# Kernel optimization log

Hardware: AMD Instinct MI355X
Metric: run time of the kernel (lower is better)

Reference implementation:

```python
import jax, jax.numpy as jnp
import numpy as np

WEIGHT_FACTOR = 1.0
N_CLUSTERS = 64


def setup_inputs() -> dict:
    key = jax.random.key(0)
    k1, k2, k3 = jax.random.split(key, 3)
    B, H, W = 128, 256, 256
    x = jax.random.uniform(k1, (B, H, W), dtype=jnp.float32)
    pattern_importance = jax.random.uniform(k2, (B, N_CLUSTERS), dtype=jnp.float32)
    # dense cluster map: value in [0, N_CLUSTERS) = cluster id; == N_CLUSTERS = unassigned (mask stays 1)
    cluster_id = jax.random.randint(k3, (H, W), 0, N_CLUSTERS + 1, dtype=jnp.int32)
    return {"x": x, "pattern_importance": pattern_importance, "cluster_id": cluster_id}


def reference(x, pattern_importance, cluster_id):
    # FFT2 over last two dims; torch fftshift with dim=None shifts ALL axes (incl. batch),
    # and jnp.fft.fftshift has the same default semantics.
    x_fft = jnp.fft.fftshift(jnp.fft.fft2(x))
    assigned = cluster_id < N_CLUSTERS                     # [H, W] bool
    cid = jnp.where(assigned, cluster_id, 0)               # safe gather index
    vals = pattern_importance[:, cid] * WEIGHT_FACTOR      # [B, H, W] gather-built mask values
    mask = jnp.where(assigned[None, :, :], vals, jnp.float32(1.0))
    x_reject = x_fft * mask
    x_ifft = jnp.abs(jnp.fft.ifft2(jnp.fft.ifftshift(x_reject)))
    x_diff = jnp.abs(x_ifft - x)
    x_new = jnp.stack([x, x_ifft, x_diff], axis=1)         # [B, 3, H, W]
    return (x_new, pattern_importance)
```

## Files before the change

### kernel.cpp

```cpp
#include <hip/hip_runtime.h>
#include <hip/hip_fp16.h>
#include <math.h>

#define BB 128
#define HH 256
#define WW 256
#define HW 65536
#define OUT_B_STRIDE 196608

__device__ __forceinline__ float2 cadd(float2 a, float2 b){ return make_float2(a.x+b.x, a.y+b.y); }
__device__ __forceinline__ float2 csub(float2 a, float2 b){ return make_float2(a.x-b.x, a.y-b.y); }

template<bool INV>
__device__ __forceinline__ float2 cmul_t(float2 a, float2 b){
  if (INV) return make_float2(a.x*b.x + a.y*b.y, a.y*b.x - a.x*b.y);
  return make_float2(a.x*b.x - a.y*b.y, a.x*b.y + a.y*b.x);
}

template<bool INV>
__device__ __forceinline__ void fft4(float2&a,float2&b,float2&c,float2&d){
  float2 t0 = cadd(a,c), t1 = csub(a,c);
  float2 t2 = cadd(b,d), t3 = csub(b,d);
  float2 t3r = INV ? make_float2(-t3.y, t3.x) : make_float2(t3.y, -t3.x);
  a = cadd(t0,t2);
  b = cadd(t1,t3r);
  c = csub(t0,t2);
  d = csub(t1,t3r);
}

template<bool INV>
__device__ __forceinline__ void fft16(float2 x[16]){
  #pragma unroll
  for (int j0=0;j0<4;++j0) fft4<INV>(x[j0], x[j0+4], x[j0+8], x[j0+12]);
  const float WR[10] = {1.f, 0.923879533f, 0.707106781f, 0.382683432f, 0.f,
                        0.f, -0.707106781f, 0.f, 0.f, -0.923879533f};
  const float WI[10] = {0.f, -0.382683432f, -0.707106781f, -0.923879533f, -1.f,
                        0.f, -0.707106781f, 0.f, 0.f, 0.382683432f};
  #pragma unroll
  for (int q0=1;q0<4;++q0)
    #pragma unroll
    for (int j0=1;j0<4;++j0){
      int k = j0*q0;
      x[j0+4*q0] = cmul_t<INV>(x[j0+4*q0], make_float2(WR[k], WI[k]));
    }
  #pragma unroll
  for (int q0=0;q0<4;++q0) fft4<INV>(x[4*q0], x[4*q0+1], x[4*q0+2], x[4*q0+3]);
  float2 t[16];
  #pragma unroll
  for (int q0=0;q0<4;++q0)
    #pragma unroll
    for (int q1=0;q1<4;++q1) t[q0+4*q1] = x[4*q0+q1];
  #pragma unroll
  for (int i=0;i<16;++i) x[i]=t[i];
}

__device__ __forceinline__ void build_tw256(float2* tw, int tid){
  float s,c;
  __sincosf(-6.28318530717958647692f * (float)tid / 256.0f, &s, &c);
  tw[tid] = make_float2(c, s);
}

__device__ __forceinline__ uint pkh2(float2 v){
  __half2 h = __float22half2_rn(v);
  return *(uint*)&h;
}
__device__ __forceinline__ float2 uph2(uint u){
  __half2 h = *(__half2*)&u;
  return __half22float2(h);
}

union SharedU {
  float  xs[16*272];
  float2 zbuf[16*273];
  float  ybuf[16*272];
};

__global__ __launch_bounds__(256, 4) void k_row_fwd(const float* __restrict__ x,
                                                    __half2* __restrict__ S,
                                                    const int* __restrict__ cid,
                                                    unsigned char* __restrict__ cidp){
  __shared__ SharedU sh;
  __shared__ float2 tw[256];
  int tid = threadIdx.x;
  int t = tid & 15, r = tid >> 4;
  build_tw256(tw, tid);

  if (blockIdx.x < 64){
    int g = (blockIdx.x*256 + tid) * 4;
    int p  = g >> 8;
    int s  = (g >> 4) & 15;
    int k1b = g & 15;
    int wfreq = 16*(p & 15) + (p >> 4);
    int w2 = (wfreq + 128) & 255;
    uchar4 v4;
    unsigned char* vp = (unsigned char*)&v4;
    #pragma unroll
    for (int i=0;i<4;++i){
      int h2 = (16*(k1b+i) + s + 128) & 255;
      int cv = cid[h2*256 + w2];
      vp[i] = (unsigned char)cv;
    }
    *(uchar4*)(cidp + g) = v4;
  }

  const float4* xb = (const float4*)x + (size_t)blockIdx.x * 1024;
  #pragma unroll
  for (int k=0;k<4;++k){
    int i2 = tid + k*256;
    float4 v = xb[i2];
    int row = i2 >> 6, c4 = i2 & 63;
    *(float4*)&sh.xs[row*272 + c4*4] = v;
  }
  __syncthreads();
  float2 X[16];
  #pragma unroll
  for (int j=0;j<16;++j) X[j] = make_float2(sh.xs[r*272 + 16*j + t], 0.f);
  __syncthreads();
  fft16<false>(X);
  #pragma unroll
  for (int q=0;q<16;++q) X[q] = cmul_t<false>(X[q], tw[t*q]);
  #pragma unroll
  for (int q=0;q<16;++q) sh.zbuf[r*273 + q*17 + t] = X[q];
  __syncthreads();
  float2 Y[16];
  #pragma unroll
  for (int tt=0;tt<16;++tt) Y[tt] = sh.zbuf[r*273 + t*17 + tt];
  fft16<false>(Y);
  int row = blockIdx.x*16 + r;
  int b = row >> 8, h = row & 255;
  uint4* dst = (uint4*)(S + (size_t)b*HW + h*256 + t*16);
  #pragma unroll
  for (int k=0;k<4;++k){
    uint4 q;
    q.x = pkh2(Y[4*k+0]); q.y = pkh2(Y[4*k+1]);
    q.z = pkh2(Y[4*k+2]); q.w = pkh2(Y[4*k+3]);
    dst[k] = q;
  }
}

__global__ __launch_bounds__(256, 4) void k_col(__half2* __restrict__ S,
                                                const unsigned char* __restrict__ cidp,
                                                const float* __restrict__ pi){
  __shared__ SharedU sh;
  __shared__ float2 tw[256];
  __shared__ float sPI[64];
  int tid = threadIdx.x;
  int c = tid & 15, t = tid >> 4;
  int cg = blockIdx.x, b = blockIdx.y;
  build_tw256(tw, tid);
  if (tid < 64) sPI[tid] = pi[(((b + 64) & 127) << 6) + tid] * 0.25f;
  __half2* Sb = S + (size_t)b*HW;
  int p = cg*16 + c;
  float2 X[16];
  #pragma unroll
  for (int j=0;j<16;++j) X[j] = uph2(*(uint*)&Sb[(16*j + t)*256 + p]);
  uint4 mq = *(const uint4*)(cidp + p*256 + t*16);
  __syncthreads();
  fft16<false>(X);
  #pragma unroll
  for (int q=0;q<16;++q) X[q] = cmul_t<false>(X[q], tw[t*q]);
  #pragma unroll
  for (int q=0;q<16;++q) sh.zbuf[c*273 + q*17 + t] = X[q];
  __syncthreads();
  int s = t;
  float2 Y[16];
  #pragma unroll
  for (int tt=0;tt<16;++tt) Y[tt] = sh.zbuf[c*273 + s*17 + tt];
  fft16<false>(Y);
  const uint* mw = (const uint*)&mq;
  #pragma unroll
  for (int k1=0;k1<16;++k1){
    int cv = (mw[k1>>2] >> ((k1&3)*8)) & 255;
    float m = (cv < 64) ? sPI[cv] : 0.25f;
    Y[k1].x *= m; Y[k1].y *= m;
  }
  __syncthreads();
  fft16<true>(Y);
  #pragma unroll
  for (int u=0;u<16;++u) Y[u] = cmul_t<true>(Y[u], tw[u*s]);
  #pragma unroll
  for (int u=0;u<16;++u) sh.zbuf[c*273 + u*17 + s] = Y[u];
  __syncthreads();
  float2 R[16];
  #pragma unroll
  for (int k0=0;k0<16;++k0) R[k0] = sh.zbuf[c*273 + t*17 + k0];
  fft16<true>(R);
  #pragma unroll
  for (int j=0;j<16;++j){
    uint u = pkh2(R[j]);
    *(uint*)&Sb[(16*j + t)*256 + p] = u;
  }
}

__global__ __launch_bounds__(256, 4) void k_row_inv_fused(const __half2* __restrict__ S,
                                                          const float* __restrict__ x,
                                                          const float* __restrict__ pi,
                                                          float* __restrict__ out){
  __shared__ SharedU sh;
  __shared__ float2 tw[256];
  int tid = threadIdx.x;
  int s = tid & 15, r = tid >> 4;
  int slice = blockIdx.x, b = blockIdx.y;
  build_tw256(tw, tid);
  int h = slice*16 + r;
  const uint4* src = (const uint4*)(S + (size_t)b*HW + h*256 + s*16);
  float2 X[16];
  #pragma unroll
  for (int k=0;k<4;++k){
    uint4 q = src[k];
    X[4*k+0] = uph2(q.x); X[4*k+1] = uph2(q.y);
    X[4*k+2] = uph2(q.z); X[4*k+3] = uph2(q.w);
  }
  __syncthreads();
  fft16<true>(X);
  #pragma unroll
  for (int u=0;u<16;++u) X[u] = cmul_t<true>(X[u], tw[u*s]);
  #pragma unroll
  for (int u=0;u<16;++u) sh.zbuf[r*273 + u*17 + s] = X[u];
  __syncthreads();
  float2 R[16];
  #pragma unroll
  for (int k0=0;k0<16;++k0) R[k0] = sh.zbuf[r*273 + s*17 + k0];
  fft16<true>(R);
  __syncthreads();
  const float scale = 1.0f/16384.0f;
  #pragma unroll
  for (int j=0;j<16;++j)
    sh.ybuf[r*272 + 16*j + s] = sqrtf(R[j].x*R[j].x + R[j].y*R[j].y) * scale;
  __syncthreads();
  const float4* x4 = (const float4*)x;
  float4* o4 = (float4*)out;
  size_t xbase = (size_t)b*16384 + slice*1024;
  size_t obase = (size_t)b*49152 + slice*1024;
  #pragma unroll
  for (int k=0;k<4;++k){
    int i2 = tid + k*256;
    int rr = i2 >> 6, c4 = i2 & 63;
    float4 y = *(float4*)&sh.ybuf[rr*272 + c4*4];
    float4 xv = x4[xbase + i2];
    float4 df;
    df.x = fabsf(y.x - xv.x); df.y = fabsf(y.y - xv.y);
    df.z = fabsf(y.z - xv.z); df.w = fabsf(y.w - xv.w);
    o4[obase + i2]         = xv;
    o4[obase + i2 + 16384] = y;
    o4[obase + i2 + 32768] = df;
  }
  if (slice == 0 && b < 8){
    const float4* p4 = (const float4*)pi;
    o4[6291456 + b*256 + tid] = p4[b*256 + tid];
  }
}

__global__ __launch_bounds__(256, 4) void k_row_inv_stage(const __half2* __restrict__ S,
                                                          float* __restrict__ out){
  __shared__ SharedU sh;
  __shared__ float2 tw[256];
  int tid = threadIdx.x;
  int s = tid & 15, r = tid >> 4;
  int slice = blockIdx.x, b = blockIdx.y;
  build_tw256(tw, tid);
  int h = slice*16 + r;
  const uint4* src = (const uint4*)(S + (size_t)b*HW + h*256 + s*16);
  float2 X[16];
  #pragma unroll
  for (int k=0;k<4;++k){
    uint4 q = src[k];
    X[4*k+0] = uph2(q.x); X[4*k+1] = uph2(q.y);
    X[4*k+2] = uph2(q.z); X[4*k+3] = uph2(q.w);
  }
  __syncthreads();
  fft16<true>(X);
  #pragma unroll
  for (int u=0;u<16;++u) X[u] = cmul_t<true>(X[u], tw[u*s]);
  #pragma unroll
  for (int u=0;u<16;++u) sh.zbuf[r*273 + u*17 + s] = X[u];
  __syncthreads();
  float2 R[16];
  #pragma unroll
  for (int k0=0;k0<16;++k0) R[k0] = sh.zbuf[r*273 + s*17 + k0];
  fft16<true>(R);
  const float scale = 1.0f/16384.0f;
  float* o = out + (size_t)b*OUT_B_STRIDE + h*256;
  #pragma unroll
  for (int j=0;j<16;++j)
    o[16*j + s] = sqrtf(R[j].x*R[j].x + R[j].y*R[j].y) * scale;
}

__global__ __launch_bounds__(256) void k_final(const float* __restrict__ x,
                                               const float* __restrict__ pi,
                                               float* __restrict__ out) {
  int i = blockIdx.x * 256 + threadIdx.x;
  const float4* x4 = (const float4*)x;
  float4* o4 = (float4*)out;
  int b = i >> 14;
  int r = i & 16383;
  int ch0 = b * 49152 + r;
  float4 y  = o4[ch0];
  float4 xv = x4[i];
  float4 df;
  df.x = fabsf(y.x - xv.x);
  df.y = fabsf(y.y - xv.y);
  df.z = fabsf(y.z - xv.z);
  df.w = fabsf(y.w - xv.w);
  o4[ch0]         = xv;
  o4[ch0 + 16384] = y;
  o4[ch0 + 32768] = df;
  if (i < 2048) {
    const float4* p4 = (const float4*)pi;
    o4[6291456 + i] = p4[i];
  }
}

extern "C" void kernel_launch(void* const* d_in, const int* in_sizes, int n_in,
                              void* d_out, int out_size, void* d_ws, size_t ws_size,
                              hipStream_t stream) {
  const float* x  = (const float*)d_in[0];
  const float* pi = (const float*)d_in[1];
  const int*  cid = (const int*)d_in[2];
  float* out = (float*)d_out;
  (void)in_sizes; (void)n_in; (void)out_size;

  const size_t S_bytes = (size_t)BB * HW * sizeof(__half2);
  const size_t cidp_bytes = 65536;

  if (ws_size >= S_bytes + cidp_bytes) {
    __half2* S = (__half2*)d_ws;
    unsigned char* cidp = (unsigned char*)d_ws + S_bytes;
    k_row_fwd<<<2048, 256, 0, stream>>>(x, S, cid, cidp);
    k_col<<<dim3(16, BB), 256, 0, stream>>>(S, cidp, pi);
    k_row_inv_fused<<<dim3(16, BB), 256, 0, stream>>>(S, x, pi, out);
  } else {
    __half2* S = (__half2*)((float*)out + HW);
    S = (__half2*)out + (size_t)BB * HW;
    unsigned char* cidp = (unsigned char*)d_ws;
    k_row_fwd<<<2048, 256, 0, stream>>>(x, S, cid, cidp);
    k_col<<<dim3(16, BB), 256, 0, stream>>>(S, cidp, pi);
    k_row_inv_stage<<<dim3(16, BB), 256, 0, stream>>>(S, out);
    k_final<<<8192, 256, 0, stream>>>(x, pi, out);
  }
}
```

Measured before the change: 176.3 us.

## Compute FFT twiddles in registers and stage transposes through half-precision LDS

Drops the shared-memory twiddle table and its build step in every FFT kernel. Twiddle factors are now made in registers from one sincos plus repeated complex multiplies. The radix-16 transpose now goes through LDS as packed half2 words instead of float2, which halves LDS traffic and footprint and removes several __syncthreads. The risks are extra precision loss from fp16 intermediates and error that builds up along the recurrence twiddles.

```diff
diff --git a/kernel.cpp b/kernel.cpp
--- a/kernel.cpp
+++ b/kernel.cpp
@@ -3,8 +3,6 @@
 #include <math.h>
 
 #define BB 128
-#define HH 256
-#define WW 256
 #define HW 65536
 #define OUT_B_STRIDE 196608
 
@@ -54,10 +52,16 @@
   for (int i=0;i<16;++i) x[i]=t[i];
 }
 
-__device__ __forceinline__ void build_tw256(float2* tw, int tid){
-  float s,c;
-  __sincosf(-6.28318530717958647692f * (float)tid / 256.0f, &s, &c);
-  tw[tid] = make_float2(c, s);
+__device__ __forceinline__ void twiddle_mul(float2 X[16], int t, float sign){
+  float sv, cv;
+  __sincosf(sign * 0.024543692606170259968f * (float)t, &sv, &cv);
+  float2 base = make_float2(cv, sv);
+  float2 f = base;
+  #pragma unroll
+  for (int q=1;q<16;++q){
+    X[q] = cmul_t<false>(X[q], f);
+    f = cmul_t<false>(f, base);
+  }
 }
 
 __device__ __forceinline__ uint pkh2(float2 v){
@@ -69,21 +73,19 @@
   return __half22float2(h);
 }
 
-union SharedU {
-  float  xs[16*272];
-  float2 zbuf[16*273];
-  float  ybuf[16*272];
+union SharedRT {
+  float xs[16*272];
+  uint  zu[16*272];
+  float yb[16*272];
 };
 
 __global__ __launch_bounds__(256, 4) void k_row_fwd(const float* __restrict__ x,
                                                     __half2* __restrict__ S,
                                                     const int* __restrict__ cid,
                                                     unsigned char* __restrict__ cidp){
-  __shared__ SharedU sh;
-  __shared__ float2 tw[256];
+  __shared__ SharedRT sh;
   int tid = threadIdx.x;
   int t = tid & 15, r = tid >> 4;
-  build_tw256(tw, tid);
 
   if (blockIdx.x < 64){
     int g = (blockIdx.x*256 + tid) * 4;
@@ -97,8 +99,7 @@
     #pragma unroll
     for (int i=0;i<4;++i){
       int h2 = (16*(k1b+i) + s + 128) & 255;
-      int cv = cid[h2*256 + w2];
-      vp[i] = (unsigned char)cv;
+      vp[i] = (unsigned char)cid[h2*256 + w2];
     }
     *(uchar4*)(cidp + g) = v4;
   }
@@ -117,14 +118,13 @@
   for (int j=0;j<16;++j) X[j] = make_float2(sh.xs[r*272 + 16*j + t], 0.f);
   __syncthreads();
   fft16<false>(X);
-  #pragma unroll
-  for (int q=0;q<16;++q) X[q] = cmul_t<false>(X[q], tw[t*q]);
-  #pragma unroll
-  for (int q=0;q<16;++q) sh.zbuf[r*273 + q*17 + t] = X[q];
+  twiddle_mul(X, t, -1.f);
+  #pragma unroll
+  for (int q=0;q<16;++q) sh.zu[r*272 + q*17 + t] = pkh2(X[q]);
   __syncthreads();
   float2 Y[16];
   #pragma unroll
-  for (int tt=0;tt<16;++tt) Y[tt] = sh.zbuf[r*273 + t*17 + tt];
+  for (int tt=0;tt<16;++tt) Y[tt] = uph2(sh.zu[r*272 + t*17 + tt]);
   fft16<false>(Y);
   int row = blockIdx.x*16 + r;
   int b = row >> 8, h = row & 255;
@@ -141,31 +141,26 @@
 __global__ __launch_bounds__(256, 4) void k_col(__half2* __restrict__ S,
                                                 const unsigned char* __restrict__ cidp,
                                                 const float* __restrict__ pi){
-  __shared__ SharedU sh;
-  __shared__ float2 tw[256];
+  __shared__ uint zu[16*274];
   __shared__ float sPI[64];
   int tid = threadIdx.x;
   int c = tid & 15, t = tid >> 4;
   int cg = blockIdx.x, b = blockIdx.y;
-  build_tw256(tw, tid);
   if (tid < 64) sPI[tid] = pi[(((b + 64) & 127) << 6) + tid] * 0.25f;
   __half2* Sb = S + (size_t)b*HW;
   int p = cg*16 + c;
   float2 X[16];
   #pragma unroll
-  for (int j=0;j<16;++j) X[j] = uph2(*(uint*)&Sb[(16*j + t)*256 + p]);
+  for (int j=0;j<16;++j) X[j] = uph2(*(const uint*)&Sb[(16*j + t)*256 + p]);
   uint4 mq = *(const uint4*)(cidp + p*256 + t*16);
-  __syncthreads();
   fft16<false>(X);
-  #pragma unroll
-  for (int q=0;q<16;++q) X[q] = cmul_t<false>(X[q], tw[t*q]);
-  #pragma unroll
-  for (int q=0;q<16;++q) sh.zbuf[c*273 + q*17 + t] = X[q];
-  __syncthreads();
-  int s = t;
+  twiddle_mul(X, t, -1.f);
+  #pragma unroll
+  for (int q=0;q<16;++q) zu[c*274 + q*17 + t] = pkh2(X[q]);
+  __syncthreads();
   float2 Y[16];
   #pragma unroll
-  for (int tt=0;tt<16;++tt) Y[tt] = sh.zbuf[c*273 + s*17 + tt];
+  for (int tt=0;tt<16;++tt) Y[tt] = uph2(zu[c*274 + t*17 + tt]);
   fft16<false>(Y);
   const uint* mw = (const uint*)&mq;
   #pragma unroll
@@ -174,34 +169,29 @@
     float m = (cv < 64) ? sPI[cv] : 0.25f;
     Y[k1].x *= m; Y[k1].y *= m;
   }
-  __syncthreads();
   fft16<true>(Y);
-  #pragma unroll
-  for (int u=0;u<16;++u) Y[u] = cmul_t<true>(Y[u], tw[u*s]);
-  #pragma unroll
-  for (int u=0;u<16;++u) sh.zbuf[c*273 + u*17 + s] = Y[u];
+  twiddle_mul(Y, t, +1.f);
+  __syncthreads();
+  #pragma unroll
+  for (int u=0;u<16;++u) zu[c*274 + u*17 + t] = pkh2(Y[u]);
   __syncthreads();
   float2 R[16];
   #pragma unroll
-  for (int k0=0;k0<16;++k0) R[k0] = sh.zbuf[c*273 + t*17 + k0];
+  for (int k0=0;k0<16;++k0) R[k0] = uph2(zu[c*274 + t*17 + k0]);
   fft16<true>(R);
   #pragma unroll
-  for (int j=0;j<16;++j){
-    uint u = pkh2(R[j]);
-    *(uint*)&Sb[(16*j + t)*256 + p] = u;
-  }
+  for (int j=0;j<16;++j)
+    *(uint*)&Sb[(16*j + t)*256 + p] = pkh2(R[j]);
 }
 
 __global__ __launch_bounds__(256, 4) void k_row_inv_fused(const __half2* __restrict__ S,
                                                           const float* __restrict__ x,
                                                           const float* __restrict__ pi,
                                                           float* __restrict__ out){
-  __shared__ SharedU sh;
-  __shared__ float2 tw[256];
+  __shared__ SharedRT sh;
   int tid = threadIdx.x;
   int s = tid & 15, r = tid >> 4;
   int slice = blockIdx.x, b = blockIdx.y;
-  build_tw256(tw, tid);
   int h = slice*16 + r;
   const uint4* src = (const uint4*)(S + (size_t)b*HW + h*256 + s*16);
   float2 X[16];
@@ -211,22 +201,20 @@
     X[4*k+0] = uph2(q.x); X[4*k+1] = uph2(q.y);
     X[4*k+2] = uph2(q.z); X[4*k+3] = uph2(q.w);
   }
-  __syncthreads();
   fft16<true>(X);
-  #pragma unroll
-  for (int u=0;u<16;++u) X[u] = cmul_t<true>(X[u], tw[u*s]);
-  #pragma unroll
-  for (int u=0;u<16;++u) sh.zbuf[r*273 + u*17 + s] = X[u];
+  twiddle_mul(X, s, +1.f);
+  #pragma unroll
+  for (int u=0;u<16;++u) sh.zu[r*272 + u*17 + s] = pkh2(X[u]);
   __syncthreads();
   float2 R[16];
   #pragma unroll
-  for (int k0=0;k0<16;++k0) R[k0] = sh.zbuf[r*273 + s*17 + k0];
+  for (int k0=0;k0<16;++k0) R[k0] = uph2(sh.zu[r*272 + s*17 + k0]);
   fft16<true>(R);
   __syncthreads();
   const float scale = 1.0f/16384.0f;
   #pragma unroll
   for (int j=0;j<16;++j)
-    sh.ybuf[r*272 + 16*j + s] = sqrtf(R[j].x*R[j].x + R[j].y*R[j].y) * scale;
+    sh.yb[r*272 + 16*j + s] = sqrtf(R[j].x*R[j].x + R[j].y*R[j].y) * scale;
   __syncthreads();
   const float4* x4 = (const float4*)x;
   float4* o4 = (float4*)out;
@@ -236,7 +224,7 @@
   for (int k=0;k<4;++k){
     int i2 = tid + k*256;
     int rr = i2 >> 6, c4 = i2 & 63;
-    float4 y = *(float4*)&sh.ybuf[rr*272 + c4*4];
+    float4 y = *(float4*)&sh.yb[rr*272 + c4*4];
     float4 xv = x4[xbase + i2];
     float4 df;
     df.x = fabsf(y.x - xv.x); df.y = fabsf(y.y - xv.y);
@@ -253,12 +241,10 @@
 
 __global__ __launch_bounds__(256, 4) void k_row_inv_stage(const __half2* __restrict__ S,
                                                           float* __restrict__ out){
-  __shared__ SharedU sh;
-  __shared__ float2 tw[256];
+  __shared__ SharedRT sh;
   int tid = threadIdx.x;
   int s = tid & 15, r = tid >> 4;
   int slice = blockIdx.x, b = blockIdx.y;
-  build_tw256(tw, tid);
   int h = slice*16 + r;
   const uint4* src = (const uint4*)(S + (size_t)b*HW + h*256 + s*16);
   float2 X[16];
@@ -268,16 +254,14 @@
     X[4*k+0] = uph2(q.x); X[4*k+1] = uph2(q.y);
     X[4*k+2] = uph2(q.z); X[4*k+3] = uph2(q.w);
   }
-  __syncthreads();
   fft16<true>(X);
-  #pragma unroll
-  for (int u=0;u<16;++u) X[u] = cmul_t<true>(X[u], tw[u*s]);
-  #pragma unroll
-  for (int u=0;u<16;++u) sh.zbuf[r*273 + u*17 + s] = X[u];
+  twiddle_mul(X, s, +1.f);
+  #pragma unroll
+  for (int u=0;u<16;++u) sh.zu[r*272 + u*17 + s] = pkh2(X[u]);
   __syncthreads();
   float2 R[16];
   #pragma unroll
-  for (int k0=0;k0<16;++k0) R[k0] = sh.zbuf[r*273 + s*17 + k0];
+  for (int k0=0;k0<16;++k0) R[k0] = uph2(sh.zu[r*272 + s*17 + k0]);
   fft16<true>(R);
   const float scale = 1.0f/16384.0f;
   float* o = out + (size_t)b*OUT_B_STRIDE + h*256;
@@ -330,8 +314,7 @@
     k_col<<<dim3(16, BB), 256, 0, stream>>>(S, cidp, pi);
     k_row_inv_fused<<<dim3(16, BB), 256, 0, stream>>>(S, x, pi, out);
   } else {
-    __half2* S = (__half2*)((float*)out + HW);
-    S = (__half2*)out + (size_t)BB * HW;
+    __half2* S = (__half2*)out + (size_t)BB * HW;
     unsigned char* cidp = (unsigned char*)d_ws;
     k_row_fwd<<<2048, 256, 0, stream>>>(x, S, cid, cidp);
     k_col<<<dim3(16, BB), 256, 0, stream>>>(S, cidp, pi);
```

Result: no change. 179.7 us (+1.9%).
